# Optimization experiments

Hardware: AMD Instinct MI355X
Metric: run time of the kernel (lower is better)

Reference implementation:

```python
import jax, jax.numpy as jnp
import numpy as np

N_NODES = 100000
N_EDGES = 3200000
IN_F, HID, N_CLS = 10, 64, 10
NEG_SLOPE = 0.01  # torch default for F.leaky_relu


def gcn_conv(h, src, dst, W, b, n_nodes):
    h = h @ W  # transform first (small feature dim -> cheap)
    # self loops
    loop = jnp.arange(n_nodes, dtype=src.dtype)
    s = jnp.concatenate([src, loop])
    d = jnp.concatenate([dst, loop])
    deg = jax.ops.segment_sum(jnp.ones_like(d, dtype=h.dtype), d, num_segments=n_nodes)
    dinv = jnp.where(deg > 0, jax.lax.rsqrt(deg), 0.0)
    norm = dinv[s] * dinv[d]  # [E+N]
    msg = h[s] * norm[:, None]  # gather + scale
    out = jax.ops.segment_sum(msg, d, num_segments=n_nodes)  # scatter-add
    return out + b


def setup_inputs() -> dict:
    key = jax.random.key(0)
    ks = jax.random.split(key, 10)
    x = jax.random.normal(ks[0], (N_NODES, IN_F), dtype=jnp.float32)
    edge_index = jax.random.randint(ks[1], (2, N_EDGES), 0, N_NODES, dtype=jnp.int64)
    def glorot(k, fan_in, fan_out):
        lim = np.sqrt(6.0 / (fan_in + fan_out))
        return jax.random.uniform(k, (fan_in, fan_out), jnp.float32, -lim, lim)
    W1 = glorot(ks[2], IN_F, HID)
    b1 = jnp.zeros((HID,), jnp.float32)
    W2 = glorot(ks[3], HID, HID)
    b2 = jnp.zeros((HID,), jnp.float32)
    W3 = glorot(ks[4], HID, HID)
    b3 = jnp.zeros((HID,), jnp.float32)
    Wfc = glorot(ks[5], HID, N_CLS)
    bfc = jnp.zeros((N_CLS,), jnp.float32)
    return {"x": x, "edge_index": edge_index, "W1": W1, "b1": b1,
            "W2": W2, "b2": b2, "W3": W3, "b3": b3, "Wfc": Wfc, "bfc": bfc}


def reference(x, edge_index, W1, b1, W2, b2, W3, b3, Wfc, bfc):
    src, dst = edge_index[0], edge_index[1]
    n = x.shape[0]
    h = jax.nn.leaky_relu(gcn_conv(x, src, dst, W1, b1, n), NEG_SLOPE)
    h = jax.nn.leaky_relu(gcn_conv(h, src, dst, W2, b2, n), NEG_SLOPE)
    h = jax.nn.leaky_relu(gcn_conv(h, src, dst, W3, b3, n), NEG_SLOPE)
    return h @ Wfc + bfc
```

## Files before the change

kernel.cpp:

```cpp
#include <hip/hip_runtime.h>
#include <hip/hip_fp16.h>

#define N_NODES_C 100000
#define N_EDGES_C 3200000
#define IN_F_C 10
#define HID_C 64
#define N_CLS_C 10
#define NEG_SLOPE_C 0.01f

#define NBUCK 98
#define BCAP  36864
#define TILE  2048

__global__ __launch_bounds__(256) void k_bucket(const int* __restrict__ src,
                                                const int* __restrict__ dst,
                                                int* __restrict__ bcur,
                                                int* __restrict__ pairs, int E) {
    __shared__ int lcnt[NBUCK];
    __shared__ int gbase[NBUCK];
    const int t = threadIdx.x;
    for (int i = t; i < NBUCK; i += 256) lcnt[i] = 0;
    __syncthreads();
    const int base = blockIdx.x * TILE;
    int p[8], r[8], nb[8];
#pragma unroll
    for (int i = 0; i < 8; ++i) {
        int e = base + t + i * 256;
        if (e < E) {
            int s = src[e], d = dst[e];
            int b = d >> 10;
            nb[i] = b;
            p[i] = (s << 10) | (d & 1023);
            r[i] = atomicAdd(&lcnt[b], 1);
        }
    }
    __syncthreads();
    for (int i = t; i < NBUCK; i += 256)
        gbase[i] = lcnt[i] ? atomicAdd(&bcur[i], lcnt[i]) : 0;
    __syncthreads();
#pragma unroll
    for (int i = 0; i < 8; ++i) {
        int e = base + t + i * 256;
        if (e < E) {
            int pos = gbase[nb[i]] + r[i];
            if (pos < BCAP) pairs[nb[i] * BCAP + pos] = p[i];
        }
    }
}

__global__ __launch_bounds__(128) void k_bscan(const int* __restrict__ bcur,
                                               int* __restrict__ bOff, int nbk) {
    __shared__ int s[128];
    int t = threadIdx.x;
    int v = (t < nbk) ? bcur[t] : 0;
    s[t] = v;
    __syncthreads();
    for (int off = 1; off < 128; off <<= 1) {
        int u = (t >= off) ? s[t - off] : 0;
        __syncthreads();
        s[t] += u;
        __syncthreads();
    }
    if (t < nbk) bOff[t] = s[t] - v;
}

__global__ __launch_bounds__(1024) void k_build(const int* __restrict__ pairs,
                                                const int* __restrict__ bcur,
                                                const int* __restrict__ bOff,
                                                int* __restrict__ row_ptr,
                                                float* __restrict__ dinv,
                                                int* __restrict__ col) {
    __shared__ int hist[1024];
    __shared__ int sm[1024];
    const int b = blockIdx.x;
    const int t = threadIdx.x;
    const int n = min(bcur[b], BCAP);
    const int base = bOff[b];
    const int* pp = pairs + b * BCAP;

    hist[t] = 0;
    __syncthreads();
    for (int i = t; i < n; i += 1024) atomicAdd(&hist[pp[i] & 1023], 1);
    __syncthreads();
    int c = hist[t];
    sm[t] = c;
    __syncthreads();
    for (int off = 1; off < 1024; off <<= 1) {
        int u = (t >= off) ? sm[t - off] : 0;
        __syncthreads();
        sm[t] += u;
        __syncthreads();
    }
    int rp = base + sm[t] - c;
    int gnode = (b << 10) + t;
    if (gnode < N_NODES_C) {
        row_ptr[gnode] = rp;
        dinv[gnode] = rsqrtf((float)(c + 1));
        if (gnode == N_NODES_C - 1) row_ptr[N_NODES_C] = rp + c;
    }
    __syncthreads();
    sm[t] = rp;
    __syncthreads();
    for (int i = t; i < n; i += 1024) {
        int p = pp[i];
        int idx = atomicAdd(&sm[p & 1023], 1);
        col[idx] = p >> 10;
    }
}

__global__ __launch_bounds__(256) void k_mm0(const float* __restrict__ x,
                                             const float* __restrict__ W,
                                             const float* __restrict__ dinv,
                                             __half* __restrict__ hs, int n) {
    __shared__ float4 W4[IN_F_C * 16];
    const int t = threadIdx.x;
    for (int i = t; i < IN_F_C * 16; i += 256) {
        int k = i >> 4, f4 = i & 15;
        W4[i] = ((const float4*)(W + k * HID_C))[f4];
    }
    __syncthreads();
    int idx = blockIdx.x * 256 + t;
    if (idx >= n * 16) return;
    int nn = idx >> 4, f4 = idx & 15;
    const float* row = x + nn * IN_F_C;
    float4 acc = make_float4(0.f, 0.f, 0.f, 0.f);
#pragma unroll
    for (int k = 0; k < IN_F_C; ++k) {
        float xv = row[k];
        float4 w = W4[k * 16 + f4];
        acc.x += xv * w.x; acc.y += xv * w.y; acc.z += xv * w.z; acc.w += xv * w.w;
    }
    float di = dinv[nn];
    __half2 h0 = __floats2half2_rn(acc.x * di, acc.y * di);
    __half2 h1 = __floats2half2_rn(acc.z * di, acc.w * di);
    ((__half2*)hs)[(nn << 5) + 2 * f4]     = h0;
    ((__half2*)hs)[(nn << 5) + 2 * f4 + 1] = h1;
}

template <int NEXT_F, bool LAST>
__global__ __launch_bounds__(256) void k_gft(const int* __restrict__ row_ptr,
                                             const int* __restrict__ col,
                                             const __half* __restrict__ hsrc,
                                             const float* __restrict__ dinv,
                                             const float* __restrict__ bias,
                                             const float* __restrict__ Wn,
                                             const float* __restrict__ bn,
                                             void* __restrict__ outp, int n) {
    __shared__ float4 Ws4[16 * NEXT_F];
    __shared__ float rowbuf[4][64];
    const int t = threadIdx.x;
    for (int i = t; i < 16 * NEXT_F; i += 256) {
        int k4 = i / NEXT_F, f = i - k4 * NEXT_F;
        Ws4[i] = make_float4(Wn[(4 * k4 + 0) * NEXT_F + f], Wn[(4 * k4 + 1) * NEXT_F + f],
                             Wn[(4 * k4 + 2) * NEXT_F + f], Wn[(4 * k4 + 3) * NEXT_F + f]);
    }
    __syncthreads();

    const int lane = t & 63;
    const int wid  = t >> 6;
    const int g    = lane >> 4;
    const int fl   = lane & 15;
    const int d = (blockIdx.x << 2) + wid;
    if (d >= n) return;
    const int beg = row_ptr[d];
    const int end = row_ptr[d + 1];
    const float2* hsv = (const float2*)hsrc;

    float4 acc = make_float4(0.f, 0.f, 0.f, 0.f);
    if (g == 0) {
        float2 raw = hsv[(d << 4) + fl];
        float2 a0 = __half22float2(*(__half2*)&raw.x);
        float2 a1 = __half22float2(*(__half2*)&raw.y);
        acc = make_float4(a0.x, a0.y, a1.x, a1.y);
    }
    int e = beg;
    for (; e + 7 < end; e += 8) {
        int s0 = col[e + g];
        int s1 = col[e + 4 + g];
        float2 r0 = hsv[(s0 << 4) + fl];
        float2 r1 = hsv[(s1 << 4) + fl];
        float2 a0 = __half22float2(*(__half2*)&r0.x);
        float2 a1 = __half22float2(*(__half2*)&r0.y);
        float2 b0 = __half22float2(*(__half2*)&r1.x);
        float2 b1 = __half22float2(*(__half2*)&r1.y);
        acc.x += a0.x + b0.x; acc.y += a0.y + b0.y;
        acc.z += a1.x + b1.x; acc.w += a1.y + b1.y;
    }
    for (; e < end; e += 4) {
        int i = e + g;
        if (i < end) {
            float2 r = hsv[(col[i] << 4) + fl];
            float2 a0 = __half22float2(*(__half2*)&r.x);
            float2 a1 = __half22float2(*(__half2*)&r.y);
            acc.x += a0.x; acc.y += a0.y; acc.z += a1.x; acc.w += a1.y;
        }
    }
    acc.x += __shfl_xor(acc.x, 16, 64); acc.y += __shfl_xor(acc.y, 16, 64);
    acc.z += __shfl_xor(acc.z, 16, 64); acc.w += __shfl_xor(acc.w, 16, 64);
    acc.x += __shfl_xor(acc.x, 32, 64); acc.y += __shfl_xor(acc.y, 32, 64);
    acc.z += __shfl_xor(acc.z, 32, 64); acc.w += __shfl_xor(acc.w, 32, 64);

    const float di = dinv[d];
    if (g == 0) {
        float4 bb = ((const float4*)bias)[fl];
        float4 v;
        v.x = acc.x * di + bb.x; v.y = acc.y * di + bb.y;
        v.z = acc.z * di + bb.z; v.w = acc.w * di + bb.w;
        v.x = v.x > 0.f ? v.x : NEG_SLOPE_C * v.x;
        v.y = v.y > 0.f ? v.y : NEG_SLOPE_C * v.y;
        v.z = v.z > 0.f ? v.z : NEG_SLOPE_C * v.z;
        v.w = v.w > 0.f ? v.w : NEG_SLOPE_C * v.w;
        ((float4*)rowbuf[wid])[fl] = v;
    }
    if (lane < NEXT_F) {
        float s = LAST ? bn[lane] : 0.f;
        const float4* rb = (const float4*)rowbuf[wid];
#pragma unroll
        for (int k4 = 0; k4 < 16; ++k4) {
            float4 r4 = rb[k4];
            float4 w4 = Ws4[k4 * NEXT_F + lane];
            s += r4.x * w4.x + r4.y * w4.y + r4.z * w4.z + r4.w * w4.w;
        }
        if (LAST) {
            ((float*)outp)[d * NEXT_F + lane] = s;
        } else {
            ((__half*)outp)[(d << 6) + lane] = __float2half(s * di);
        }
    }
}

extern "C" void kernel_launch(void* const* d_in, const int* in_sizes, int n_in,
                              void* d_out, int out_size, void* d_ws, size_t ws_size,
                              hipStream_t stream) {
    const float* x   = (const float*)d_in[0];
    const int*   ei  = (const int*)d_in[1];
    const float* W1  = (const float*)d_in[2];
    const float* b1  = (const float*)d_in[3];
    const float* W2  = (const float*)d_in[4];
    const float* b2  = (const float*)d_in[5];
    const float* W3  = (const float*)d_in[6];
    const float* b3  = (const float*)d_in[7];
    const float* Wfc = (const float*)d_in[8];
    const float* bfc = (const float*)d_in[9];
    float* out = (float*)d_out;

    const int N = N_NODES_C;
    const int E = N_EDGES_C;
    const int* src = ei;
    const int* dst = ei + E;

    float*  dinv    = (float*)d_ws;
    int*    bcur    = (int*)(dinv + N);
    int*    bOff    = bcur + 128;
    int*    row_ptr = bOff + 128;
    int*    col     = row_ptr + N + 4;
    int*    pairs   = col + E;
    __half* hsA     = (__half*)pairs;
    __half* hsB     = (__half*)(pairs + (size_t)NBUCK * BCAP);

    int gN4  = (N + 3) / 4;
    int gM0  = (N * 16 + 255) / 256;
    int gBK  = (E + TILE - 1) / TILE;

    hipMemsetAsync(bcur, 0, 128 * sizeof(int), stream);
    k_bucket<<<gBK, 256, 0, stream>>>(src, dst, bcur, pairs, E);
    k_bscan<<<1, 128, 0, stream>>>(bcur, bOff, NBUCK);
    k_build<<<NBUCK, 1024, 0, stream>>>(pairs, bcur, bOff, row_ptr, dinv, col);

    k_mm0<<<gM0, 256, 0, stream>>>(x, W1, dinv, hsA, N);

    k_gft<HID_C, false><<<gN4, 256, 0, stream>>>(row_ptr, col, hsA, dinv, b1, W2, nullptr, hsB, N);
    k_gft<HID_C, false><<<gN4, 256, 0, stream>>>(row_ptr, col, hsB, dinv, b2, W3, nullptr, hsA, N);
    k_gft<N_CLS_C, true><<<gN4, 256, 0, stream>>>(row_ptr, col, hsA, dinv, b3, Wfc, bfc, out, N);
}
```

Measured before the change: 446.0 us.

## Restructure GCN aggregation: two rows per wave, fp16 dot2 transform, fused prep and scan

Each wave in the aggregation kernels now processes two destination rows and gathers 16 edges per batch, so more memory loads are in flight. The hidden-layer transform uses fp16 weights prepacked by a new prep kernel and computed with fdot2. The bucket scan is folded into the build kernel and the memset is folded into the prep kernel, which removes two launches. This adds register pressure and uses fp16 for the products, which may cost some accuracy.

```diff
diff --git a/kernel.cpp b/kernel.cpp
--- a/kernel.cpp
+++ b/kernel.cpp
@@ -11,6 +11,46 @@
 #define NBUCK 98
 #define BCAP  36864
 #define TILE  2048
+
+typedef _Float16 f16x2 __attribute__((ext_vector_type(2)));
+
+__device__ __forceinline__ float fdot2(unsigned int a, unsigned int b, float c) {
+#if defined(__has_builtin) && __has_builtin(__builtin_amdgcn_fdot2)
+    return __builtin_amdgcn_fdot2(__builtin_bit_cast(f16x2, a), __builtin_bit_cast(f16x2, b), c, false);
+#else
+    __half2 ah = __builtin_bit_cast(__half2, a), bh = __builtin_bit_cast(__half2, b);
+    float2 af = __half22float2(ah), bf = __half22float2(bh);
+    return c + af.x * bf.x + af.y * bf.y;
+#endif
+}
+
+__global__ __launch_bounds__(256) void k_prep(const float* __restrict__ W2, const float* __restrict__ W3,
+                                              const float* __restrict__ Wfc,
+                                              uint4* __restrict__ wh2, uint4* __restrict__ wh3,
+                                              float4* __restrict__ wfq, int* __restrict__ bcur) {
+    const int b = blockIdx.x, t = threadIdx.x;
+    if (b < 2) {
+        const float* W = b ? W3 : W2;
+        uint4* wh = b ? wh3 : wh2;
+        for (int i = t; i < 8 * HID_C; i += 256) {
+            int k8 = i >> 6, f = i & 63;
+            __half2 h[4];
+#pragma unroll
+            for (int j = 0; j < 4; ++j)
+                h[j] = __floats2half2_rn(W[(8 * k8 + 2 * j) * HID_C + f],
+                                         W[(8 * k8 + 2 * j + 1) * HID_C + f]);
+            wh[i] = *(uint4*)h;
+        }
+    } else if (b == 2) {
+        if (t < 16 * N_CLS_C) {
+            int k4 = t / N_CLS_C, f = t - k4 * N_CLS_C;
+            wfq[t] = make_float4(Wfc[(4 * k4 + 0) * N_CLS_C + f], Wfc[(4 * k4 + 1) * N_CLS_C + f],
+                                 Wfc[(4 * k4 + 2) * N_CLS_C + f], Wfc[(4 * k4 + 3) * N_CLS_C + f]);
+        }
+    } else {
+        if (t < 128) bcur[t] = 0;
+    }
+}
 
 __global__ __launch_bounds__(256) void k_bucket(const int* __restrict__ src,
                                                 const int* __restrict__ dst,
@@ -48,35 +88,29 @@
     }
 }
 
-__global__ __launch_bounds__(128) void k_bscan(const int* __restrict__ bcur,
-                                               int* __restrict__ bOff, int nbk) {
-    __shared__ int s[128];
-    int t = threadIdx.x;
-    int v = (t < nbk) ? bcur[t] : 0;
-    s[t] = v;
-    __syncthreads();
-    for (int off = 1; off < 128; off <<= 1) {
-        int u = (t >= off) ? s[t - off] : 0;
-        __syncthreads();
-        s[t] += u;
-        __syncthreads();
-    }
-    if (t < nbk) bOff[t] = s[t] - v;
-}
-
 __global__ __launch_bounds__(1024) void k_build(const int* __restrict__ pairs,
                                                 const int* __restrict__ bcur,
-                                                const int* __restrict__ bOff,
                                                 int* __restrict__ row_ptr,
                                                 float* __restrict__ dinv,
                                                 int* __restrict__ col) {
     __shared__ int hist[1024];
     __shared__ int sm[1024];
+    __shared__ int bs[128];
     const int b = blockIdx.x;
     const int t = threadIdx.x;
     const int n = min(bcur[b], BCAP);
-    const int base = bOff[b];
     const int* pp = pairs + b * BCAP;
+
+    if (t < 128) bs[t] = (t < NBUCK) ? bcur[t] : 0;
+    __syncthreads();
+    for (int off = 1; off < 128; off <<= 1) {
+        int u = 0;
+        if (t < 128 && t >= off) u = bs[t - off];
+        __syncthreads();
+        if (t < 128) bs[t] += u;
+        __syncthreads();
+    }
+    const int base = (b > 0) ? bs[b - 1] : 0;
 
     hist[t] = 0;
     __syncthreads();
@@ -131,102 +165,220 @@
         acc.x += xv * w.x; acc.y += xv * w.y; acc.z += xv * w.z; acc.w += xv * w.w;
     }
     float di = dinv[nn];
-    __half2 h0 = __floats2half2_rn(acc.x * di, acc.y * di);
-    __half2 h1 = __floats2half2_rn(acc.z * di, acc.w * di);
-    ((__half2*)hs)[(nn << 5) + 2 * f4]     = h0;
-    ((__half2*)hs)[(nn << 5) + 2 * f4 + 1] = h1;
-}
-
-template <int NEXT_F, bool LAST>
-__global__ __launch_bounds__(256) void k_gft(const int* __restrict__ row_ptr,
+    ((__half2*)hs)[(nn << 5) + 2 * f4]     = __floats2half2_rn(acc.x * di, acc.y * di);
+    ((__half2*)hs)[(nn << 5) + 2 * f4 + 1] = __floats2half2_rn(acc.z * di, acc.w * di);
+}
+
+#define GBATCH(e, acc)                                                                 \
+    {                                                                                  \
+        int s0 = col[(e) + g], s1 = col[(e) + 4 + g];                                  \
+        int s2 = col[(e) + 8 + g], s3 = col[(e) + 12 + g];                             \
+        float2 r0 = hsv[(s0 << 4) + fl], r1 = hsv[(s1 << 4) + fl];                     \
+        float2 r2 = hsv[(s2 << 4) + fl], r3 = hsv[(s3 << 4) + fl];                     \
+        float2 x0 = __half22float2(*(__half2*)&r0.x), x1 = __half22float2(*(__half2*)&r0.y); \
+        float2 y0 = __half22float2(*(__half2*)&r1.x), y1 = __half22float2(*(__half2*)&r1.y); \
+        float2 z0 = __half22float2(*(__half2*)&r2.x), z1 = __half22float2(*(__half2*)&r2.y); \
+        float2 w0 = __half22float2(*(__half2*)&r3.x), w1 = __half22float2(*(__half2*)&r3.y); \
+        acc.x += (x0.x + y0.x) + (z0.x + w0.x);                                        \
+        acc.y += (x0.y + y0.y) + (z0.y + w0.y);                                        \
+        acc.z += (x1.x + y1.x) + (z1.x + w1.x);                                        \
+        acc.w += (x1.y + y1.y) + (z1.y + w1.y);                                        \
+    }
+
+#define GBATCH2(e0, e1, acc0, acc1)                                                    \
+    {                                                                                  \
+        int a0 = col[(e0) + g], a1 = col[(e0) + 4 + g];                                \
+        int a2 = col[(e0) + 8 + g], a3 = col[(e0) + 12 + g];                           \
+        int b0 = col[(e1) + g], b1 = col[(e1) + 4 + g];                                \
+        int b2 = col[(e1) + 8 + g], b3 = col[(e1) + 12 + g];                           \
+        float2 r0 = hsv[(a0 << 4) + fl], r1 = hsv[(a1 << 4) + fl];                     \
+        float2 r2 = hsv[(a2 << 4) + fl], r3 = hsv[(a3 << 4) + fl];                     \
+        float2 q0 = hsv[(b0 << 4) + fl], q1 = hsv[(b1 << 4) + fl];                     \
+        float2 q2 = hsv[(b2 << 4) + fl], q3 = hsv[(b3 << 4) + fl];                     \
+        float2 x0 = __half22float2(*(__half2*)&r0.x), x1 = __half22float2(*(__half2*)&r0.y); \
+        float2 y0 = __half22float2(*(__half2*)&r1.x), y1 = __half22float2(*(__half2*)&r1.y); \
+        float2 z0 = __half22float2(*(__half2*)&r2.x), z1 = __half22float2(*(__half2*)&r2.y); \
+        float2 w0 = __half22float2(*(__half2*)&r3.x), w1 = __half22float2(*(__half2*)&r3.y); \
+        acc0.x += (x0.x + y0.x) + (z0.x + w0.x);                                       \
+        acc0.y += (x0.y + y0.y) + (z0.y + w0.y);                                       \
+        acc0.z += (x1.x + y1.x) + (z1.x + w1.x);                                       \
+        acc0.w += (x1.y + y1.y) + (z1.y + w1.y);                                       \
+        x0 = __half22float2(*(__half2*)&q0.x); x1 = __half22float2(*(__half2*)&q0.y);  \
+        y0 = __half22float2(*(__half2*)&q1.x); y1 = __half22float2(*(__half2*)&q1.y);  \
+        z0 = __half22float2(*(__half2*)&q2.x); z1 = __half22float2(*(__half2*)&q2.y);  \
+        w0 = __half22float2(*(__half2*)&q3.x); w1 = __half22float2(*(__half2*)&q3.y);  \
+        acc1.x += (x0.x + y0.x) + (z0.x + w0.x);                                       \
+        acc1.y += (x0.y + y0.y) + (z0.y + w0.y);                                       \
+        acc1.z += (x1.x + y1.x) + (z1.x + w1.x);                                       \
+        acc1.w += (x1.y + y1.y) + (z1.y + w1.y);                                       \
+    }
+
+#define GTAIL(e, endv, acc)                                                            \
+    for (; (e) < (endv); (e) += 4) {                                                   \
+        int i = (e) + g;                                                               \
+        if (i < (endv)) {                                                              \
+            float2 r = hsv[(col[i] << 4) + fl];                                        \
+            float2 u0 = __half22float2(*(__half2*)&r.x);                               \
+            float2 u1 = __half22float2(*(__half2*)&r.y);                               \
+            acc.x += u0.x; acc.y += u0.y; acc.z += u1.x; acc.w += u1.y;                \
+        }                                                                              \
+    }
+
+#define GREDUCE(acc)                                                                   \
+    acc.x += __shfl_xor(acc.x, 16, 64); acc.y += __shfl_xor(acc.y, 16, 64);            \
+    acc.z += __shfl_xor(acc.z, 16, 64); acc.w += __shfl_xor(acc.w, 16, 64);            \
+    acc.x += __shfl_xor(acc.x, 32, 64); acc.y += __shfl_xor(acc.y, 32, 64);            \
+    acc.z += __shfl_xor(acc.z, 32, 64); acc.w += __shfl_xor(acc.w, 32, 64);
+
+#define GSELF(d, acc)                                                                  \
+    if (g == 0 && (d) < n) {                                                           \
+        float2 raw = hsv[((d) << 4) + fl];                                             \
+        float2 l0 = __half22float2(*(__half2*)&raw.x);                                 \
+        float2 l1 = __half22float2(*(__half2*)&raw.y);                                 \
+        acc = make_float4(l0.x, l0.y, l1.x, l1.y);                                     \
+    }
+
+__global__ __launch_bounds__(512) void k_gft(const int* __restrict__ row_ptr,
                                              const int* __restrict__ col,
                                              const __half* __restrict__ hsrc,
                                              const float* __restrict__ dinv,
                                              const float* __restrict__ bias,
-                                             const float* __restrict__ Wn,
+                                             const uint4* __restrict__ wh,
+                                             __half* __restrict__ hnext, int n) {
+    __shared__ uint4 WhL[8 * HID_C];
+    __shared__ __half2 rowh[8][32];
+    const int t = threadIdx.x;
+    WhL[t] = wh[t];
+    __syncthreads();
+
+    const int lane = t & 63, wid = t >> 6;
+    const int g = lane >> 4, fl = lane & 15;
+    const int d0 = (blockIdx.x << 4) + wid;
+    const int d1 = d0 + 8;
+    const float2* hsv = (const float2*)hsrc;
+
+    int e0 = 0, end0 = -1, e1 = 0, end1 = -1;
+    if (d0 < n) { e0 = row_ptr[d0]; end0 = row_ptr[d0 + 1]; }
+    if (d1 < n) { e1 = row_ptr[d1]; end1 = row_ptr[d1 + 1]; }
+
+    float4 acc0 = make_float4(0.f, 0.f, 0.f, 0.f), acc1 = acc0;
+    GSELF(d0, acc0)
+    GSELF(d1, acc1)
+
+    while (e0 + 15 < end0 && e1 + 15 < end1) {
+        GBATCH2(e0, e1, acc0, acc1)
+        e0 += 16; e1 += 16;
+    }
+    for (; e0 + 15 < end0; e0 += 16) GBATCH(e0, acc0)
+    for (; e1 + 15 < end1; e1 += 16) GBATCH(e1, acc1)
+    GTAIL(e0, end0, acc0)
+    GTAIL(e1, end1, acc1)
+    GREDUCE(acc0)
+    GREDUCE(acc1)
+
+#define EPI_XFORM(d, acc)                                                              \
+    if ((d) < n) {                                                                     \
+        const float di = dinv[d];                                                      \
+        if (g == 0) {                                                                  \
+            float4 bb = ((const float4*)bias)[fl];                                     \
+            float4 v;                                                                  \
+            v.x = acc.x * di + bb.x; v.y = acc.y * di + bb.y;                          \
+            v.z = acc.z * di + bb.z; v.w = acc.w * di + bb.w;                          \
+            v.x = v.x > 0.f ? v.x : NEG_SLOPE_C * v.x;                                 \
+            v.y = v.y > 0.f ? v.y : NEG_SLOPE_C * v.y;                                 \
+            v.z = v.z > 0.f ? v.z : NEG_SLOPE_C * v.z;                                 \
+            v.w = v.w > 0.f ? v.w : NEG_SLOPE_C * v.w;                                 \
+            rowh[wid][2 * fl]     = __floats2half2_rn(v.x, v.y);                       \
+            rowh[wid][2 * fl + 1] = __floats2half2_rn(v.z, v.w);                       \
+        }                                                                              \
+        float s = 0.f;                                                                 \
+        const uint4* rq = (const uint4*)rowh[wid];                                     \
+        _Pragma("unroll")                                                              \
+        for (int k8 = 0; k8 < 8; ++k8) {                                               \
+            uint4 wv = WhL[(k8 << 6) + lane];                                          \
+            uint4 rv = rq[k8];                                                         \
+            s = fdot2(rv.x, wv.x, s);                                                  \
+            s = fdot2(rv.y, wv.y, s);                                                  \
+            s = fdot2(rv.z, wv.z, s);                                                  \
+            s = fdot2(rv.w, wv.w, s);                                                  \
+        }                                                                              \
+        hnext[((d) << 6) + lane] = __float2half(s * di);                               \
+    }
+
+    EPI_XFORM(d0, acc0)
+    EPI_XFORM(d1, acc1)
+#undef EPI_XFORM
+}
+
+__global__ __launch_bounds__(512) void k_gfc(const int* __restrict__ row_ptr,
+                                             const int* __restrict__ col,
+                                             const __half* __restrict__ hsrc,
+                                             const float* __restrict__ dinv,
+                                             const float* __restrict__ bias,
+                                             const float4* __restrict__ wq,
                                              const float* __restrict__ bn,
-                                             void* __restrict__ outp, int n) {
-    __shared__ float4 Ws4[16 * NEXT_F];
-    __shared__ float rowbuf[4][64];
+                                             float* __restrict__ out, int n) {
+    __shared__ float4 Ws4[16 * N_CLS_C];
+    __shared__ float rowbuf[8][64];
     const int t = threadIdx.x;
-    for (int i = t; i < 16 * NEXT_F; i += 256) {
-        int k4 = i / NEXT_F, f = i - k4 * NEXT_F;
-        Ws4[i] = make_float4(Wn[(4 * k4 + 0) * NEXT_F + f], Wn[(4 * k4 + 1) * NEXT_F + f],
-                             Wn[(4 * k4 + 2) * NEXT_F + f], Wn[(4 * k4 + 3) * NEXT_F + f]);
-    }
-    __syncthreads();
-
-    const int lane = t & 63;
-    const int wid  = t >> 6;
-    const int g    = lane >> 4;
-    const int fl   = lane & 15;
-    const int d = (blockIdx.x << 2) + wid;
-    if (d >= n) return;
-    const int beg = row_ptr[d];
-    const int end = row_ptr[d + 1];
+    if (t < 16 * N_CLS_C) Ws4[t] = wq[t];
+    __syncthreads();
+
+    const int lane = t & 63, wid = t >> 6;
+    const int g = lane >> 4, fl = lane & 15;
+    const int d0 = (blockIdx.x << 4) + wid;
+    const int d1 = d0 + 8;
     const float2* hsv = (const float2*)hsrc;
 
-    float4 acc = make_float4(0.f, 0.f, 0.f, 0.f);
-    if (g == 0) {
-        float2 raw = hsv[(d << 4) + fl];
-        float2 a0 = __half22float2(*(__half2*)&raw.x);
-        float2 a1 = __half22float2(*(__half2*)&raw.y);
-        acc = make_float4(a0.x, a0.y, a1.x, a1.y);
-    }
-    int e = beg;
-    for (; e + 7 < end; e += 8) {
-        int s0 = col[e + g];
-        int s1 = col[e + 4 + g];
-        float2 r0 = hsv[(s0 << 4) + fl];
-        float2 r1 = hsv[(s1 << 4) + fl];
-        float2 a0 = __half22float2(*(__half2*)&r0.x);
-        float2 a1 = __half22float2(*(__half2*)&r0.y);
-        float2 b0 = __half22float2(*(__half2*)&r1.x);
-        float2 b1 = __half22float2(*(__half2*)&r1.y);
-        acc.x += a0.x + b0.x; acc.y += a0.y + b0.y;
-        acc.z += a1.x + b1.x; acc.w += a1.y + b1.y;
-    }
-    for (; e < end; e += 4) {
-        int i = e + g;
-        if (i < end) {
-            float2 r = hsv[(col[i] << 4) + fl];
-            float2 a0 = __half22float2(*(__half2*)&r.x);
-            float2 a1 = __half22float2(*(__half2*)&r.y);
-            acc.x += a0.x; acc.y += a0.y; acc.z += a1.x; acc.w += a1.y;
-        }
-    }
-    acc.x += __shfl_xor(acc.x, 16, 64); acc.y += __shfl_xor(acc.y, 16, 64);
-    acc.z += __shfl_xor(acc.z, 16, 64); acc.w += __shfl_xor(acc.w, 16, 64);
-    acc.x += __shfl_xor(acc.x, 32, 64); acc.y += __shfl_xor(acc.y, 32, 64);
-    acc.z += __shfl_xor(acc.z, 32, 64); acc.w += __shfl_xor(acc.w, 32, 64);
-
-    const float di = dinv[d];
-    if (g == 0) {
-        float4 bb = ((const float4*)bias)[fl];
-        float4 v;
-        v.x = acc.x * di + bb.x; v.y = acc.y * di + bb.y;
-        v.z = acc.z * di + bb.z; v.w = acc.w * di + bb.w;
-        v.x = v.x > 0.f ? v.x : NEG_SLOPE_C * v.x;
-        v.y = v.y > 0.f ? v.y : NEG_SLOPE_C * v.y;
-        v.z = v.z > 0.f ? v.z : NEG_SLOPE_C * v.z;
-        v.w = v.w > 0.f ? v.w : NEG_SLOPE_C * v.w;
-        ((float4*)rowbuf[wid])[fl] = v;
-    }
-    if (lane < NEXT_F) {
-        float s = LAST ? bn[lane] : 0.f;
-        const float4* rb = (const float4*)rowbuf[wid];
-#pragma unroll
-        for (int k4 = 0; k4 < 16; ++k4) {
-            float4 r4 = rb[k4];
-            float4 w4 = Ws4[k4 * NEXT_F + lane];
-            s += r4.x * w4.x + r4.y * w4.y + r4.z * w4.z + r4.w * w4.w;
-        }
-        if (LAST) {
-            ((float*)outp)[d * NEXT_F + lane] = s;
-        } else {
-            ((__half*)outp)[(d << 6) + lane] = __float2half(s * di);
-        }
-    }
+    int e0 = 0, end0 = -1, e1 = 0, end1 = -1;
+    if (d0 < n) { e0 = row_ptr[d0]; end0 = row_ptr[d0 + 1]; }
+    if (d1 < n) { e1 = row_ptr[d1]; end1 = row_ptr[d1 + 1]; }
+
+    float4 acc0 = make_float4(0.f, 0.f, 0.f, 0.f), acc1 = acc0;
+    GSELF(d0, acc0)
+    GSELF(d1, acc1)
+
+    while (e0 + 15 < end0 && e1 + 15 < end1) {
+        GBATCH2(e0, e1, acc0, acc1)
+        e0 += 16; e1 += 16;
+    }
+    for (; e0 + 15 < end0; e0 += 16) GBATCH(e0, acc0)
+    for (; e1 + 15 < end1; e1 += 16) GBATCH(e1, acc1)
+    GTAIL(e0, end0, acc0)
+    GTAIL(e1, end1, acc1)
+    GREDUCE(acc0)
+    GREDUCE(acc1)
+
+#define EPI_FC(d, acc)                                                                 \
+    if ((d) < n) {                                                                     \
+        const float di = dinv[d];                                                      \
+        if (g == 0) {                                                                  \
+            float4 bb = ((const float4*)bias)[fl];                                     \
+            float4 v;                                                                  \
+            v.x = acc.x * di + bb.x; v.y = acc.y * di + bb.y;                          \
+            v.z = acc.z * di + bb.z; v.w = acc.w * di + bb.w;                          \
+            v.x = v.x > 0.f ? v.x : NEG_SLOPE_C * v.x;                                 \
+            v.y = v.y > 0.f ? v.y : NEG_SLOPE_C * v.y;                                 \
+            v.z = v.z > 0.f ? v.z : NEG_SLOPE_C * v.z;                                 \
+            v.w = v.w > 0.f ? v.w : NEG_SLOPE_C * v.w;                                 \
+            ((float4*)rowbuf[wid])[fl] = v;                                            \
+        }                                                                              \
+        if (lane < N_CLS_C) {                                                          \
+            float s = bn[lane];                                                        \
+            const float4* rb = (const float4*)rowbuf[wid];                             \
+            _Pragma("unroll")                                                          \
+            for (int k4 = 0; k4 < 16; ++k4) {                                          \
+                float4 r4 = rb[k4];                                                    \
+                float4 w4 = Ws4[k4 * N_CLS_C + lane];                                  \
+                s += r4.x * w4.x + r4.y * w4.y + r4.z * w4.z + r4.w * w4.w;            \
+            }                                                                          \
+            out[(d) * N_CLS_C + lane] = s;                                             \
+        }                                                                              \
+    }
+
+    EPI_FC(d0, acc0)
+    EPI_FC(d1, acc1)
+#undef EPI_FC
 }
 
 extern "C" void kernel_launch(void* const* d_in, const int* in_sizes, int n_in,
@@ -251,25 +403,27 @@
 
     float*  dinv    = (float*)d_ws;
     int*    bcur    = (int*)(dinv + N);
-    int*    bOff    = bcur + 128;
-    int*    row_ptr = bOff + 128;
-    int*    col     = row_ptr + N + 4;
+    int*    row_ptr = bcur + 128;
+    uint4*  wh2     = (uint4*)(row_ptr + N + 4);
+    uint4*  wh3     = wh2 + 512;
+    float4* wfcq    = (float4*)(wh3 + 512);
+    int*    col     = (int*)(wfcq + 160);
     int*    pairs   = col + E;
     __half* hsA     = (__half*)pairs;
     __half* hsB     = (__half*)(pairs + (size_t)NBUCK * BCAP);
 
-    int gN4  = (N + 3) / 4;
+    int gN16 = (N + 15) / 16;
     int gM0  = (N * 16 + 255) / 256;
     int gBK  = (E + TILE - 1) / TILE;
 
-    hipMemsetAsync(bcur, 0, 128 * sizeof(int), stream);
+    k_prep<<<4, 256, 0, stream>>>(W2, W3, Wfc, wh2, wh3, wfcq, bcur);
+
     k_bucket<<<gBK, 256, 0, stream>>>(src, dst, bcur, pairs, E);
-    k_bscan<<<1, 128, 0, stream>>>(bcur, bOff, NBUCK);
-    k_build<<<NBUCK, 1024, 0, stream>>>(pairs, bcur, bOff, row_ptr, dinv, col);
+    k_build<<<NBUCK, 1024, 0, stream>>>(pairs, bcur, row_ptr, dinv, col);
 
     k_mm0<<<gM0, 256, 0, stream>>>(x, W1, dinv, hsA, N);
 
-    k_gft<HID_C, false><<<gN4, 256, 0, stream>>>(row_ptr, col, hsA, dinv, b1, W2, nullptr, hsB, N);
-    k_gft<HID_C, false><<<gN4, 256, 0, stream>>>(row_ptr, col, hsB, dinv, b2, W3, nullptr, hsA, N);
-    k_gft<N_CLS_C, true><<<gN4, 256, 0, stream>>>(row_ptr, col, hsA, dinv, b3, Wfc, bfc, out, N);
-}
+    k_gft<<<gN16, 512, 0, stream>>>(row_ptr, col, hsA, dinv, b1, wh2, hsB, N);
+    k_gft<<<gN16, 512, 0, stream>>>(row_ptr, col, hsB, dinv, b2, wh3, hsA, N);
+    k_gfc<<<gN16, 512, 0, stream>>>(row_ptr, col, hsA, dinv, b3, wfcq, bfc, out, N);
+}
```

Result: faster. 403.1 us (-9.6%).
